# Optimization experiments

Measured on AMD Instinct MI355X. Metric: run time of the kernel, lower is better.

The kernel has to match this reference:

```python
import jax, jax.numpy as jnp
import numpy as np

N = 50000          # nodes
E = 1_000_000      # edges
NODE_DIM = 16
EMB = 64           # embed_dim
OUT = 64           # out_dim per head
EA_DIM = 8         # raw edge_attr_dim
HEADS = 8
SLOPE = 0.01       # leaky_relu default negative slope
LN_EPS = 1e-5


def mlp(x, w, b, g, beta):
    # MLP(in, out): Linear -> LayerNorm -> ReLU (standard block in this repo)
    y = x @ w + b
    mu = jnp.mean(y, axis=-1, keepdims=True)
    var = jnp.var(y, axis=-1, keepdims=True)
    y = (y - mu) / jnp.sqrt(var + LN_EPS) * g + beta
    return jax.nn.relu(y)


def gat_layer(x, ea, src, tgt, W, a):
    """AA_GATlayer forward (dropout = identity at eval).
    x: [N, in], ea: [E, EMB], W: [in, OUT], a: [2*OUT + EMB]."""
    h = x @ W                                  # [N, OUT]
    d = h.shape[1]
    a_src, a_tgt, a_edge = a[:d], a[d:2 * d], a[2 * d:]
    # score = leaky_relu(a @ concat([h_src, h_tgt, ea])) without materializing the concat
    s = jax.nn.leaky_relu(h[src] @ a_src + h[tgt] @ a_tgt + ea @ a_edge, SLOPE)  # [E]
    s = s - jnp.max(s)
    e = jnp.exp(s)
    denom = jax.ops.segment_sum(e, src, num_segments=N)          # [N]
    attn = e / (denom[src] + 1e-16)                              # [E]
    h_prime = jax.ops.segment_sum(h[tgt] * attn[:, None], src, num_segments=N)  # [N, OUT]
    return jax.nn.elu(h_prime)


def setup_inputs() -> dict:
    key = jax.random.key(0)
    ks = jax.random.split(key, 16)
    sc = lambda fan_in: 1.0 / np.sqrt(fan_in)
    inp = {}
    inp["X"] = jax.random.normal(ks[0], (N, NODE_DIM), jnp.float32)
    inp["edge_attr"] = jax.random.normal(ks[1], (E, EA_DIM), jnp.float32)
    inp["edge_index"] = jax.random.randint(ks[2], (2, E), 0, N, jnp.int64)
    inp["matched_car_infra_nodes"] = jax.random.randint(ks[3], (1000,), 0, N, jnp.int64)
    # node_embed MLP params
    inp["w_node"] = jax.random.uniform(ks[4], (NODE_DIM, EMB), jnp.float32, -sc(NODE_DIM), sc(NODE_DIM))
    inp["b_node"] = jnp.zeros((EMB,), jnp.float32)
    inp["g_node"] = jnp.ones((EMB,), jnp.float32)
    inp["beta_node"] = jnp.zeros((EMB,), jnp.float32)
    # edge_attr_embed MLP params
    inp["w_edge"] = jax.random.uniform(ks[5], (EA_DIM, EMB), jnp.float32, -sc(EA_DIM), sc(EA_DIM))
    inp["b_edge"] = jnp.zeros((EMB,), jnp.float32)
    inp["g_edge"] = jnp.ones((EMB,), jnp.float32)
    inp["beta_edge"] = jnp.zeros((EMB,), jnp.float32)
    # 8 GAT heads: W [EMB,OUT], a [2*OUT+EMB]
    inp["gat_W"] = jax.random.uniform(ks[6], (HEADS, EMB, OUT), jnp.float32, -sc(EMB), sc(EMB))
    inp["gat_a"] = jax.random.uniform(ks[7], (HEADS, 2 * OUT + EMB), jnp.float32, -sc(2 * OUT + EMB), sc(2 * OUT + EMB))
    # output GAT layer: W [OUT*HEADS, OUT], a [2*OUT+EMB]
    inp["out_W"] = jax.random.uniform(ks[8], (OUT * HEADS, OUT), jnp.float32, -sc(OUT * HEADS), sc(OUT * HEADS))
    inp["out_a"] = jax.random.uniform(ks[9], (2 * OUT + EMB,), jnp.float32, -sc(2 * OUT + EMB), sc(2 * OUT + EMB))
    return inp


def reference(X, edge_attr, w_node, b_node, g_node, beta_node,
              w_edge, b_edge, g_edge, beta_edge,
              gat_W, gat_a, out_W, out_a,
              edge_index, matched_car_infra_nodes):
    src, tgt = edge_index[0], edge_index[1]
    x = mlp(X, w_node, b_node, g_node, beta_node)                  # [N, EMB]
    ea = mlp(edge_attr, w_edge, b_edge, g_edge, beta_edge)         # [E, EMB]
    heads = [gat_layer(x, ea, src, tgt, gat_W[i], gat_a[i]) for i in range(HEADS)]
    xh = jax.nn.elu(jnp.concatenate(heads, axis=1))                # [N, OUT*HEADS]
    out = gat_layer(xh, ea, src, tgt, out_W, out_a)                # [N, OUT]
    return jax.nn.log_softmax(out, axis=1)
```

## Files before the change

kernel.cpp:

```cpp
#include <hip/hip_runtime.h>
#include <hip/hip_fp16.h>

#define NN 50000
#define EE 1000000
#define HALF 25000
#define EPT 4

typedef _Float16 h8v __attribute__((ext_vector_type(8)));
typedef float    f4a __attribute__((ext_vector_type(4)));
typedef float    f4v __attribute__((ext_vector_type(4)));

__device__ __forceinline__ float wsum(float v){
#pragma unroll
  for(int m=1;m<64;m<<=1) v += __shfl_xor(v,m,64);
  return v;
}
__device__ __forceinline__ unsigned encf(float f){
  unsigned u = __float_as_uint(f);
  return (u & 0x80000000u) ? ~u : (u | 0x80000000u);
}
__device__ __forceinline__ float decf(unsigned u){
  u = (u & 0x80000000u) ? (u & 0x7fffffffu) : ~u;
  return __uint_as_float(u);
}

__global__ __launch_bounds__(256) void zero_k(int* counts, int* cursor, unsigned* mx){
  int i = blockIdx.x*blockDim.x + threadIdx.x;
  if(i < NN){ counts[i] = 0; cursor[i] = 0; }
  if(i < 64) mx[i] = 0u;
}

__global__ __launch_bounds__(64) void cvec_k(const float* __restrict__ gat_W, const float* __restrict__ gat_a,
                                             float* __restrict__ cdir){
  int h = blockIdx.x, k = threadIdx.x;
  const float* W = gat_W + (size_t)h*64*64;
  const float* a = gat_a + (size_t)h*192;
  float cs = 0.f, ct = 0.f;
#pragma unroll
  for(int j=0;j<64;j++){ float wv = W[k*64+j]; cs += wv*a[j]; ct += wv*a[64+j]; }
  cdir[h*64 + k]       = cs;
  cdir[512 + h*64 + k] = ct;
}

__global__ __launch_bounds__(256) void cvtw_k(const float* __restrict__ gat_W, const float* __restrict__ out_W,
                                              __half* __restrict__ WT, __half* __restrict__ OT){
  int h = blockIdx.x; int tid = threadIdx.x;
  for(int idx = tid; idx < 4096; idx += 256){
    int j = idx >> 6, k = idx & 63;
    WT[(size_t)h*4096 + k*64 + j] = __float2half(gat_W[(size_t)h*4096 + j*64 + k]);
    OT[(size_t)h*4096 + k*64 + j] = __float2half(out_W[(size_t)h*4096 + j*64 + k]);
  }
}

__global__ __launch_bounds__(256) void node_mlp(const float* __restrict__ X, const float* __restrict__ w,
                                                const float* __restrict__ b, const float* __restrict__ g,
                                                const float* __restrict__ beta, const float* __restrict__ cdir,
                                                __half* __restrict__ x, float* __restrict__ ps8,
                                                float* __restrict__ pt8){
  int wid  = (blockIdx.x*blockDim.x + threadIdx.x) >> 6;
  int lane = threadIdx.x & 63;
  if(wid >= NN) return;
  float acc = b[lane];
#pragma unroll
  for(int k=0;k<16;k++) acc += X[wid*16+k] * w[k*64+lane];
  float mu  = wsum(acc) * (1.0f/64.0f);
  float d   = acc - mu;
  float var = wsum(d*d) * (1.0f/64.0f);
  float y   = d * rsqrtf(var + 1e-5f) * g[lane] + beta[lane];
  float xv  = fmaxf(y, 0.0f);
  x[(size_t)wid*64 + lane] = __float2half(xv);
#pragma unroll 1
  for(int h=0;h<8;h++){
    float a = wsum(xv * cdir[h*64+lane]);
    float c = wsum(xv * cdir[512 + h*64+lane]);
    if(lane == 0){ ps8[wid*8+h] = a; pt8[wid*8+h] = c; }
  }
}

__global__ __launch_bounds__(256) void hist_k(const int* __restrict__ src, int* __restrict__ counts){
  int e = blockIdx.x*blockDim.x + threadIdx.x;
  if(e < EE){
    int s = src[e];
    if((unsigned)s >= NN) s = 0;
    atomicAdd(&counts[s], 1);
  }
}

__global__ __launch_bounds__(256) void scan1_k(const int* __restrict__ counts, int* __restrict__ bsum){
  int i = blockIdx.x*256 + threadIdx.x;
  int v = (i < NN) ? counts[i] : 0;
  int s = v;
#pragma unroll
  for(int m=1;m<64;m<<=1) s += __shfl_xor(s,m,64);
  __shared__ int sm[4];
  if((threadIdx.x & 63) == 0) sm[threadIdx.x>>6] = s;
  __syncthreads();
  if(threadIdx.x == 0) bsum[blockIdx.x] = sm[0]+sm[1]+sm[2]+sm[3];
}

__global__ __launch_bounds__(256) void scan2_k(const int* __restrict__ bsum, int* __restrict__ bpre,
                                               int* __restrict__ offs){
  const int NB = (NN + 255)/256;
  int t = threadIdx.x;
  __shared__ int sm[256];
  int v = (t < NB) ? bsum[t] : 0;
  sm[t] = v; __syncthreads();
  for(int off=1; off<256; off<<=1){
    int u = (t >= off) ? sm[t-off] : 0;
    __syncthreads();
    sm[t] += u;
    __syncthreads();
  }
  if(t < NB) bpre[t] = sm[t] - v;
  if(t == 0) offs[NN] = EE;
}

__global__ __launch_bounds__(256) void scan3_k(const int* __restrict__ counts, const int* __restrict__ bpre,
                                               int* __restrict__ offs){
  int i = blockIdx.x*256 + threadIdx.x;
  int t = threadIdx.x;
  __shared__ int sm[256];
  int v = (i < NN) ? counts[i] : 0;
  sm[t] = v; __syncthreads();
  for(int off=1; off<256; off<<=1){
    int u = (t >= off) ? sm[t-off] : 0;
    __syncthreads();
    sm[t] += u;
    __syncthreads();
  }
  if(i < NN) offs[i] = bpre[blockIdx.x] + sm[t] - v;
}

__global__ __launch_bounds__(256) void scatter_k(const int* __restrict__ src, const int* __restrict__ tgt,
                                                 const int* __restrict__ offs, int* __restrict__ cursor,
                                                 int* __restrict__ rank, int* __restrict__ tgt_s,
                                                 int* __restrict__ src_s){
  int e = blockIdx.x*blockDim.x + threadIdx.x;
  if(e < EE){
    int s = src[e];
    if((unsigned)s >= NN) s = 0;
    int pos = offs[s] + atomicAdd(&cursor[s], 1);
    rank[e] = pos;
    int t = tgt[e];
    if((unsigned)t >= NN) t = 0;
    tgt_s[pos] = t;
    src_s[pos] = s;
  }
}

__global__ __launch_bounds__(256, 1) void edge_mlp_q(const int* __restrict__ rank, const float* __restrict__ ea,
                                                  const float* __restrict__ w, const float* __restrict__ b,
                                                  const float* __restrict__ g, const float* __restrict__ beta,
                                                  const float* __restrict__ gat_a, const float* __restrict__ out_a,
                                                  __half* __restrict__ q8h, float* __restrict__ q_out,
                                                  unsigned* __restrict__ mx){
  __shared__ float P[64*20];
  __shared__ float smx[4][9];
  int tid = threadIdx.x;
  for(int idx=tid; idx<1280; idx+=256){
    int j = idx/20, c = idx - j*20;
    float v;
    if(c < 8)       v = w[c*64+j];
    else if(c == 8) v = b[j];
    else if(c == 9) v = g[j];
    else if(c ==10) v = beta[j];
    else if(c ==11) v = out_a[128+j];
    else            v = gat_a[(c-12)*192 + 128 + j];
    P[idx] = v;
  }
  __syncthreads();
  int base = blockIdx.x*(256*EPT) + tid;
  float4 ia[EPT], ib[EPT];
  bool  vl[EPT];
#pragma unroll
  for(int k=0;k<EPT;k++){
    int e = base + k*256;
    vl[k] = (e < EE);
    size_t es = vl[k] ? (size_t)e : 0;
    ia[k] = ((const float4*)ea)[es*2];
    ib[k] = ((const float4*)ea)[es*2+1];
  }
  float s1[EPT], s2[EPT];
#pragma unroll
  for(int k=0;k<EPT;k++){ s1[k]=0.f; s2[k]=0.f; }
#pragma unroll 4
  for(int j=0;j<64;j++){
    float4 w0 = *(const float4*)&P[j*20];
    float4 w1 = *(const float4*)&P[j*20+4];
    float4 c4 = *(const float4*)&P[j*20+8];
#pragma unroll
    for(int k=0;k<EPT;k++){
      float acc = c4.x;
      acc = fmaf(ia[k].x,w0.x, fmaf(ia[k].y,w0.y, fmaf(ia[k].z,w0.z, fmaf(ia[k].w,w0.w, acc))));
      acc = fmaf(ib[k].x,w1.x, fmaf(ib[k].y,w1.y, fmaf(ib[k].z,w1.z, fmaf(ib[k].w,w1.w, acc))));
      s1[k] += acc;
      s2[k] = fmaf(acc,acc,s2[k]);
    }
  }
  float mu[EPT], inv[EPT];
#pragma unroll
  for(int k=0;k<EPT;k++){
    mu[k]  = s1[k]*(1.0f/64.0f);
    float var = fmaxf(s2[k]*(1.0f/64.0f) - mu[k]*mu[k], 0.0f);
    inv[k] = rsqrtf(var + 1e-5f);
  }
  float qv[EPT][9];
#pragma unroll
  for(int k=0;k<EPT;k++)
#pragma unroll
    for(int r=0;r<9;r++) qv[k][r]=0.f;
#pragma unroll 4
  for(int j=0;j<64;j++){
    float4 w0 = *(const float4*)&P[j*20];
    float4 w1 = *(const float4*)&P[j*20+4];
    float4 c4 = *(const float4*)&P[j*20+8];
    float4 a0 = *(const float4*)&P[j*20+12];
    float4 a1 = *(const float4*)&P[j*20+16];
#pragma unroll
    for(int k=0;k<EPT;k++){
      float acc = c4.x;
      acc = fmaf(ia[k].x,w0.x, fmaf(ia[k].y,w0.y, fmaf(ia[k].z,w0.z, fmaf(ia[k].w,w0.w, acc))));
      acc = fmaf(ib[k].x,w1.x, fmaf(ib[k].y,w1.y, fmaf(ib[k].z,w1.z, fmaf(ib[k].w,w1.w, acc))));
      float yj = fmaxf(fmaf((acc - mu[k])*inv[k], c4.y, c4.z), 0.0f);
      qv[k][0]=fmaf(yj,a0.x,qv[k][0]); qv[k][1]=fmaf(yj,a0.y,qv[k][1]);
      qv[k][2]=fmaf(yj,a0.z,qv[k][2]); qv[k][3]=fmaf(yj,a0.w,qv[k][3]);
      qv[k][4]=fmaf(yj,a1.x,qv[k][4]); qv[k][5]=fmaf(yj,a1.y,qv[k][5]);
      qv[k][6]=fmaf(yj,a1.z,qv[k][6]); qv[k][7]=fmaf(yj,a1.w,qv[k][7]);
      qv[k][8]=fmaf(yj,c4.w,qv[k][8]);
    }
  }
  float mq[9];
#pragma unroll
  for(int r=0;r<9;r++) mq[r] = -3.0e38f;
#pragma unroll
  for(int k=0;k<EPT;k++){
    if(vl[k]){
      int e = base + k*256;
      int rk = rank[e];
      __half2 p01 = __floats2half2_rn(qv[k][0],qv[k][1]);
      __half2 p23 = __floats2half2_rn(qv[k][2],qv[k][3]);
      __half2 p45 = __floats2half2_rn(qv[k][4],qv[k][5]);
      __half2 p67 = __floats2half2_rn(qv[k][6],qv[k][7]);
      uint4 pk;
      pk.x = *(unsigned*)&p01; pk.y = *(unsigned*)&p23;
      pk.z = *(unsigned*)&p45; pk.w = *(unsigned*)&p67;
      *(uint4*)(q8h + (size_t)rk*8) = pk;
      q_out[rk] = qv[k][8];
#pragma unroll
      for(int r=0;r<9;r++) mq[r] = fmaxf(mq[r], qv[k][r]);
    }
  }
#pragma unroll
  for(int r=0;r<9;r++)
#pragma unroll
    for(int m=1;m<64;m<<=1) mq[r] = fmaxf(mq[r], __shfl_xor(mq[r],m,64));
  int wv = tid>>6, lane = tid&63;
  if(lane == 0){
#pragma unroll
    for(int r=0;r<9;r++) smx[wv][r] = mq[r];
  }
  __syncthreads();
  if(tid < 9){
    float v = fmaxf(fmaxf(smx[0][tid],smx[1][tid]), fmaxf(smx[2][tid],smx[3][tid]));
    atomicMax(&mx[tid], encf(v));
  }
}

__global__ __launch_bounds__(256) void maxp_k(const float* __restrict__ ps8, const float* __restrict__ pt8,
                                              unsigned* __restrict__ mx){
  float m[16];
#pragma unroll
  for(int r=0;r<16;r++) m[r] = -3.0e38f;
  for(int i = blockIdx.x*256 + threadIdx.x; i < NN; i += gridDim.x*256){
    float4 a = ((const float4*)ps8)[(size_t)i*2];
    float4 c = ((const float4*)ps8)[(size_t)i*2+1];
    float4 d = ((const float4*)pt8)[(size_t)i*2];
    float4 e = ((const float4*)pt8)[(size_t)i*2+1];
    m[0]=fmaxf(m[0],a.x); m[1]=fmaxf(m[1],a.y); m[2]=fmaxf(m[2],a.z); m[3]=fmaxf(m[3],a.w);
    m[4]=fmaxf(m[4],c.x); m[5]=fmaxf(m[5],c.y); m[6]=fmaxf(m[6],c.z); m[7]=fmaxf(m[7],c.w);
    m[8]=fmaxf(m[8],d.x); m[9]=fmaxf(m[9],d.y); m[10]=fmaxf(m[10],d.z); m[11]=fmaxf(m[11],d.w);
    m[12]=fmaxf(m[12],e.x); m[13]=fmaxf(m[13],e.y); m[14]=fmaxf(m[14],e.z); m[15]=fmaxf(m[15],e.w);
  }
#pragma unroll
  for(int r=0;r<16;r++)
#pragma unroll
    for(int msk=1;msk<64;msk<<=1) m[r] = fmaxf(m[r], __shfl_xor(m[r],msk,64));
  __shared__ float sm[4][16];
  int wv = threadIdx.x>>6, lane = threadIdx.x&63;
  if(lane == 0){
#pragma unroll
    for(int r=0;r<16;r++) sm[wv][r] = m[r];
  }
  __syncthreads();
  if(threadIdx.x < 16){
    int r = threadIdx.x;
    float v = fmaxf(fmaxf(sm[0][r],sm[1][r]), fmaxf(sm[2][r],sm[3][r]));
    atomicMax(&mx[16+r], encf(v));
  }
}

__global__ __launch_bounds__(256) void maxpo_k(const float* __restrict__ ps_o, const float* __restrict__ pt_o,
                                               unsigned* __restrict__ mx){
  float m0 = -3.0e38f, m1 = -3.0e38f;
  for(int i = blockIdx.x*256 + threadIdx.x; i < NN; i += gridDim.x*256){
    m0 = fmaxf(m0, ps_o[i]); m1 = fmaxf(m1, pt_o[i]);
  }
#pragma unroll
  for(int msk=1;msk<64;msk<<=1){ m0=fmaxf(m0,__shfl_xor(m0,msk,64)); m1=fmaxf(m1,__shfl_xor(m1,msk,64)); }
  __shared__ float sm[4][2];
  int wv = threadIdx.x>>6, lane = threadIdx.x&63;
  if(lane == 0){ sm[wv][0]=m0; sm[wv][1]=m1; }
  __syncthreads();
  if(threadIdx.x < 2){
    int r = threadIdx.x;
    float v = fmaxf(fmaxf(sm[0][r],sm[1][r]), fmaxf(sm[2][r],sm[3][r]));
    atomicMax(&mx[32+r], encf(v));
  }
}

__global__ __launch_bounds__(256) void score_k(const int* __restrict__ src_s, const int* __restrict__ tgt_s,
                                               const float* __restrict__ ps8, const float* __restrict__ pt8,
                                               const unsigned* __restrict__ mx, const __half* __restrict__ q8h,
                                               __half* __restrict__ w8h){
  int i = blockIdx.x*256 + threadIdx.x;
  if(i >= EE) return;
  int s = src_s[i], t = tgt_s[i];
  uint4 rq = *(const uint4*)(q8h + (size_t)i*8);
  float2 q01 = __half22float2(*(const __half2*)&rq.x);
  float2 q23 = __half22float2(*(const __half2*)&rq.y);
  float2 q45 = __half22float2(*(const __half2*)&rq.z);
  float2 q67 = __half22float2(*(const __half2*)&rq.w);
  float4 sa = ((const float4*)ps8)[(size_t)s*2];
  float4 sb = ((const float4*)ps8)[(size_t)s*2+1];
  float4 ta = ((const float4*)pt8)[(size_t)t*2];
  float4 tb = ((const float4*)pt8)[(size_t)t*2+1];
  float sv[8] = {q01.x+sa.x+ta.x, q01.y+sa.y+ta.y, q23.x+sa.z+ta.z, q23.y+sa.w+ta.w,
                 q45.x+sb.x+tb.x, q45.y+sb.y+tb.y, q67.x+sb.z+tb.z, q67.y+sb.w+tb.w};
  float wv[8];
#pragma unroll
  for(int h=0;h<8;h++){
    float B = decf(mx[h]) + decf(mx[16+h]) + decf(mx[24+h]);
    float M = (B > 0.f) ? B : 0.01f*B;
    float x = sv[h];
    x = (x > 0.f) ? x : 0.01f*x;
    wv[h] = __expf(x - M);
  }
  __half2 p01 = __floats2half2_rn(wv[0],wv[1]);
  __half2 p23 = __floats2half2_rn(wv[2],wv[3]);
  __half2 p45 = __floats2half2_rn(wv[4],wv[5]);
  __half2 p67 = __floats2half2_rn(wv[6],wv[7]);
  uint4 pk;
  pk.x = *(unsigned*)&p01; pk.y = *(unsigned*)&p23;
  pk.z = *(unsigned*)&p45; pk.w = *(unsigned*)&p67;
  *(uint4*)(w8h + (size_t)i*8) = pk;
}

__global__ __launch_bounds__(256) void agg_k(const int* __restrict__ offs, const int* __restrict__ tgt_s,
    const __half* __restrict__ w8h, const __half* __restrict__ x, __half* __restrict__ pre, int nbase){
  int wid  = nbase + ((blockIdx.x*blockDim.x + threadIdx.x) >> 6);
  int lane = threadIdx.x & 63;
  int quad = lane >> 4, l16 = lane & 15;
  int b  = offs[wid];
  int e2 = offs[wid+1];
  float  den[8];
  float4 num[8];
#pragma unroll
  for(int h=0;h<8;h++){ den[h] = 0.f; num[h] = make_float4(0.f,0.f,0.f,0.f); }
  for(int i=b+quad; i<e2; i+=4){
    int t = tgt_s[i];
    uint4 rw = *(const uint4*)(w8h + (size_t)i*8);
    float2 w01 = __half22float2(*(const __half2*)&rw.x);
    float2 w23 = __half22float2(*(const __half2*)&rw.y);
    float2 w45 = __half22float2(*(const __half2*)&rw.z);
    float2 w67 = __half22float2(*(const __half2*)&rw.w);
    uint2 raw = *(const uint2*)(x + (size_t)t*64 + l16*4);
    float2 fa = __half22float2(*(const __half2*)&raw.x);
    float2 fb = __half22float2(*(const __half2*)&raw.y);
    float4 xv = make_float4(fa.x, fa.y, fb.x, fb.y);
    float wv[8] = {w01.x,w01.y,w23.x,w23.y, w45.x,w45.y,w67.x,w67.y};
#pragma unroll
    for(int h=0;h<8;h++){
      den[h]   += wv[h];
      num[h].x = fmaf(wv[h],xv.x,num[h].x); num[h].y = fmaf(wv[h],xv.y,num[h].y);
      num[h].z = fmaf(wv[h],xv.z,num[h].z); num[h].w = fmaf(wv[h],xv.w,num[h].w);
    }
  }
#pragma unroll
  for(int h=0;h<8;h++){
    den[h]   += __shfl_xor(den[h],16,64);   den[h]   += __shfl_xor(den[h],32,64);
    num[h].x += __shfl_xor(num[h].x,16,64); num[h].x += __shfl_xor(num[h].x,32,64);
    num[h].y += __shfl_xor(num[h].y,16,64); num[h].y += __shfl_xor(num[h].y,32,64);
    num[h].z += __shfl_xor(num[h].z,16,64); num[h].z += __shfl_xor(num[h].z,32,64);
    num[h].w += __shfl_xor(num[h].w,16,64); num[h].w += __shfl_xor(num[h].w,32,64);
  }
  __half* dst = pre + (size_t)(wid - nbase)*512;
#pragma unroll
  for(int k=0;k<2;k++){
    int h = 2*quad + k;
    float invd = (den[h] > 0.f) ? 1.0f/den[h] : 0.f;
    __half2 h0 = __floats2half2_rn(num[h].x*invd, num[h].y*invd);
    __half2 h1 = __floats2half2_rn(num[h].z*invd, num[h].w*invd);
    uint2 pk; pk.x = *(unsigned*)&h0; pk.y = *(unsigned*)&h1;
    *(uint2*)(dst + h*64 + l16*4) = pk;
  }
}

__global__ __launch_bounds__(256) void transform_mfma(const __half* __restrict__ pre,
                                                      const __half* __restrict__ WT,
                                                      const __half* __restrict__ OT,
                                                      float* __restrict__ h2p,
                                                      int nbase, int cn){
  __shared__ __half zl[4*16*64];
  int tid = threadIdx.x;
  int w  = tid >> 6, l = tid & 63;
  int lr = l & 15, lg = l >> 4;
  int n0 = blockIdx.x * 64;
  int g  = blockIdx.y;
  h2p += (size_t)g * NN * 64;
  int gn  = n0 + w*16 + lr;
  int gnr = (gn < cn) ? gn : 0;
  __half* zw = zl + w*1024;
  f4a out[4];
#pragma unroll
  for(int i=0;i<4;i++){ out[i][0]=0.f; out[i][1]=0.f; out[i][2]=0.f; out[i][3]=0.f; }
#pragma unroll 1
  for(int hh=0; hh<4; hh++){
    int h = g*4 + hh;
    h8v a1_0 = *(const h8v*)(pre + (size_t)gnr*512 + h*64 + 0*32 + lg*8);
    h8v a1_1 = *(const h8v*)(pre + (size_t)gnr*512 + h*64 + 1*32 + lg*8);
    f4a zacc[4];
#pragma unroll
    for(int nt=0; nt<4; nt++){ zacc[nt][0]=0.f; zacc[nt][1]=0.f; zacc[nt][2]=0.f; zacc[nt][3]=0.f; }
    const __half* WTh = WT + (size_t)h*4096;
#pragma unroll
    for(int nt=0; nt<4; nt++){
      h8v b0 = *(const h8v*)(WTh + (nt*16 + lr)*64 + 0*32 + lg*8);
      h8v b1 = *(const h8v*)(WTh + (nt*16 + lr)*64 + 1*32 + lg*8);
      zacc[nt] = __builtin_amdgcn_mfma_f32_16x16x32_f16(a1_0, b0, zacc[nt], 0, 0, 0);
      zacc[nt] = __builtin_amdgcn_mfma_f32_16x16x32_f16(a1_1, b1, zacc[nt], 0, 0, 0);
    }
#pragma unroll
    for(int nt=0; nt<4; nt++){
#pragma unroll
      for(int r=0; r<4; r++){
        float v = zacc[nt][r];
        float z = (v > 0.f) ? v : expm1f(v);
        z = (z > 0.f) ? z : expm1f(z);
        int rho = lg*4 + r;
        int c   = nt*16 + lr;
        int pc  = (((c>>3) ^ (rho&7))<<3) | (c&7);
        zw[rho*64 + pc] = __float2half(z);
      }
    }
    const __half* OTh = OT + (size_t)h*4096;
#pragma unroll
    for(int ks=0; ks<2; ks++){
      int Gp = (lg + 4*ks) ^ (lr & 7);
      h8v a2 = *(const h8v*)(zw + lr*64 + Gp*8);
#pragma unroll
      for(int nt=0; nt<4; nt++){
        h8v b2 = *(const h8v*)(OTh + (nt*16 + lr)*64 + ks*32 + lg*8);
        out[nt] = __builtin_amdgcn_mfma_f32_16x16x32_f16(a2, b2, out[nt], 0, 0, 0);
      }
    }
  }
#pragma unroll
  for(int nt=0; nt<4; nt++){
#pragma unroll
    for(int r=0; r<4; r++){
      int grow = n0 + w*16 + lg*4 + r;
      if(grow < cn) h2p[(size_t)(nbase + grow)*64 + nt*16 + lr] = out[nt][r];
    }
  }
}

__global__ __launch_bounds__(256) void finalize_po(const float* __restrict__ p0, const float* __restrict__ p1,
                                                   const float* __restrict__ out_a, __half* __restrict__ h2f,
                                                   float* __restrict__ ps_o, float* __restrict__ pt_o){
  int wid  = (blockIdx.x*blockDim.x + threadIdx.x) >> 6;
  int lane = threadIdx.x & 63;
  if(wid >= NN) return;
  float v = p0[(size_t)wid*64 + lane] + p1[(size_t)wid*64 + lane];
  float ps = wsum(v * out_a[lane]);
  float pt = wsum(v * out_a[64+lane]);
  if(lane == 0){ ps_o[wid] = ps; pt_o[wid] = pt; }
  h2f[(size_t)wid*64 + lane] = __float2half(v);
}

__global__ __launch_bounds__(256) void agg_out(const int* __restrict__ offs, const int* __restrict__ tgt_s,
                                               const float* __restrict__ q_out, const float* __restrict__ ps_o,
                                               const float* __restrict__ pt_o, const unsigned* __restrict__ mx,
                                               const __half* __restrict__ h2f, float* __restrict__ dout){
  int wid  = (blockIdx.x*blockDim.x + threadIdx.x) >> 6;
  int lane = threadIdx.x & 63;
  if(wid >= NN) return;
  int quad = lane >> 4, l16 = lane & 15;
  int b  = offs[wid];
  int e2 = offs[wid+1];
  float B = decf(mx[8]) + decf(mx[32]) + decf(mx[33]);
  float M = (B > 0.f) ? B : 0.01f*B;
  float pso = ps_o[wid];
  float4 num = make_float4(0.f,0.f,0.f,0.f);
  float den = 0.f;
  for(int i=b+quad; i<e2; i+=4){
    int t = tgt_s[i];
    float sv = q_out[i] + pso + pt_o[t];
    sv = (sv > 0.f) ? sv : 0.01f*sv;
    float w = __expf(sv - M);
    uint2 raw = *(const uint2*)(h2f + (size_t)t*64 + l16*4);
    float2 fa = __half22float2(*(const __half2*)&raw.x);
    float2 fb = __half22float2(*(const __half2*)&raw.y);
    den += w;
    num.x = fmaf(w,fa.x,num.x); num.y = fmaf(w,fa.y,num.y);
    num.z = fmaf(w,fb.x,num.z); num.w = fmaf(w,fb.y,num.w);
  }
  den   += __shfl_xor(den,16,64);   den   += __shfl_xor(den,32,64);
  num.x += __shfl_xor(num.x,16,64); num.x += __shfl_xor(num.x,32,64);
  num.y += __shfl_xor(num.y,16,64); num.y += __shfl_xor(num.y,32,64);
  num.z += __shfl_xor(num.z,16,64); num.z += __shfl_xor(num.z,32,64);
  num.w += __shfl_xor(num.w,16,64); num.w += __shfl_xor(num.w,32,64);
  float inv = (den > 0.f) ? 1.0f/den : 0.f;
  float z[4];
  float mloc = -3.0e38f;
#pragma unroll
  for(int k=0;k<4;k++){
    float hp = ((&num.x)[k]) * inv;
    z[k] = (hp > 0.f) ? hp : expm1f(hp);
    mloc = fmaxf(mloc, z[k]);
  }
#pragma unroll
  for(int msk=1; msk<16; msk<<=1) mloc = fmaxf(mloc, __shfl_xor(mloc,msk,64));
  float ssum = 0.f;
#pragma unroll
  for(int k=0;k<4;k++) ssum += __expf(z[k] - mloc);
#pragma unroll
  for(int msk=1; msk<16; msk<<=1) ssum += __shfl_xor(ssum,msk,64);
  float lse = mloc + logf(ssum);
  if(quad == 0){
    f4v o; o.x = z[0]-lse; o.y = z[1]-lse; o.z = z[2]-lse; o.w = z[3]-lse;
    __builtin_nontemporal_store(o, (f4v*)(dout + (size_t)wid*64 + l16*4));
  }
}

extern "C" void kernel_launch(void* const* d_in, const int* in_sizes, int n_in,
                              void* d_out, int out_size, void* d_ws, size_t ws_size,
                              hipStream_t stream) {
  const float* X         = (const float*)d_in[0];
  const float* edge_attr = (const float*)d_in[1];
  const int*   edge_index= (const int*)d_in[2];
  const float* w_node    = (const float*)d_in[4];
  const float* b_node    = (const float*)d_in[5];
  const float* g_node    = (const float*)d_in[6];
  const float* beta_node = (const float*)d_in[7];
  const float* w_edge    = (const float*)d_in[8];
  const float* b_edge    = (const float*)d_in[9];
  const float* g_edge    = (const float*)d_in[10];
  const float* beta_edge = (const float*)d_in[11];
  const float* gat_W     = (const float*)d_in[12];
  const float* gat_a     = (const float*)d_in[13];
  const float* out_W     = (const float*)d_in[14];
  const float* out_a     = (const float*)d_in[15];
  float* dout = (float*)d_out;

  const int* src = edge_index;
  const int* tgt = edge_index + EE;

  char* base = (char*)d_ws;
  size_t off = 0;
  auto take = [&](size_t bytes)->char*{ char* p = base + off; off += (bytes + 31) & ~(size_t)31; return p; };
  int*      counts = (int*)     take((size_t)NN*4);
  int*      cursor = (int*)     take((size_t)NN*4);
  int*      offs   = (int*)     take((size_t)(NN+1)*4);
  int*      bsum   = (int*)     take(256*4);
  int*      bpre   = (int*)     take(256*4);
  unsigned* mx     = (unsigned*)take(64*4);
  float*    ps_o   = (float*)   take((size_t)NN*4);
  float*    pt_o   = (float*)   take((size_t)NN*4);
  float*    cdir   = (float*)   take(1024*4);
  int*      rank   = (int*)     take((size_t)EE*4);
  int*      tgt_s  = (int*)     take((size_t)EE*4);
  int*      src_s  = (int*)     take((size_t)EE*4);
  float*    ps8    = (float*)   take((size_t)NN*8*4);
  float*    pt8    = (float*)   take((size_t)NN*8*4);
  __half*   xh     = (__half*)  take((size_t)NN*64*2);
  __half*   h2fh   = (__half*)  take((size_t)NN*64*2);
  __half*   WT16   = (__half*)  take((size_t)8*4096*2);
  __half*   OT16   = (__half*)  take((size_t)8*4096*2);
  float*    h2p    = (float*)   take((size_t)2*NN*64*4);
  __half*   q8h    = (__half*)  take((size_t)EE*8*2);
  __half*   w8h    = (__half*)  take((size_t)EE*8*2);
  float*    q_out  = (float*)   take((size_t)EE*4);
  __half*   pre    = (__half*)  take((size_t)HALF*512*2);

  const int NBLK_N  = (NN*64 + 255)/256;
  const int NBLK_E  = (EE + 255)/256;
  const int NBLK_EM = (EE + 256*EPT - 1)/(256*EPT);
  const int NBLK_S  = (NN + 255)/256;
  const int NBLK_A  = HALF/4;
  const int NBLK_T  = (HALF + 63)/64;

  zero_k   <<<NBLK_S, 256, 0, stream>>>(counts, cursor, mx);
  cvec_k   <<<8,       64, 0, stream>>>(gat_W, gat_a, cdir);
  cvtw_k   <<<8,      256, 0, stream>>>(gat_W, out_W, WT16, OT16);
  node_mlp <<<NBLK_N, 256, 0, stream>>>(X, w_node, b_node, g_node, beta_node, cdir, xh, ps8, pt8);
  hist_k   <<<NBLK_E, 256, 0, stream>>>(src, counts);
  scan1_k  <<<NBLK_S, 256, 0, stream>>>(counts, bsum);
  scan2_k  <<<1,      256, 0, stream>>>(bsum, bpre, offs);
  scan3_k  <<<NBLK_S, 256, 0, stream>>>(counts, bpre, offs);
  scatter_k<<<NBLK_E, 256, 0, stream>>>(src, tgt, offs, cursor, rank, tgt_s, src_s);
  edge_mlp_q<<<NBLK_EM,256, 0, stream>>>(rank, edge_attr, w_edge, b_edge, g_edge, beta_edge,
                                        gat_a, out_a, q8h, q_out, mx);
  maxp_k   <<<128,    256, 0, stream>>>(ps8, pt8, mx);
  score_k  <<<NBLK_E, 256, 0, stream>>>(src_s, tgt_s, ps8, pt8, mx, q8h, w8h);

  for(int half=0; half<2; half++){
    int nbase = half*HALF;
    agg_k<<<NBLK_A, 256, 0, stream>>>(offs, tgt_s, w8h, xh, pre, nbase);
    dim3 tg((unsigned)NBLK_T, 2);
    transform_mfma<<<tg, 256, 0, stream>>>(pre, WT16, OT16, h2p, nbase, HALF);
  }

  finalize_po<<<NBLK_N, 256, 0, stream>>>(h2p, h2p + (size_t)NN*64, out_a, h2fh, ps_o, pt_o);
  maxpo_k    <<<128,  256, 0, stream>>>(ps_o, pt_o, mx);
  agg_out    <<<NBLK_N,256, 0, stream>>>(offs, tgt_s, q_out, ps_o, pt_o, mx, h2fh, dout);
}
```

Before: 686.8 us.

## Merge prep kernels, fuse node MLP with histogram, single-block scan, unsplit aggregation

Folds the zero, cvec and weight-transpose kernels into one prep kernel. It also fuses node_mlp with the edge histogram in a single launch and replaces the three-pass scan with one 1024-thread block scan. The two-half agg/transform loop becomes one pass over all nodes, using a full-size pre buffer, and edge_mlp_q launch bounds are relaxed to allow two blocks per CU. Together these cut launch count and serial gaps, at the cost of a larger workspace (about 51MB for pre) and a scan that runs on a single block.

```diff
diff --git a/kernel.cpp b/kernel.cpp
--- a/kernel.cpp
+++ b/kernel.cpp
@@ -3,7 +3,6 @@
 
 #define NN 50000
 #define EE 1000000
-#define HALF 25000
 #define EPT 4
 
 typedef _Float16 h8v __attribute__((ext_vector_type(8)));
@@ -24,40 +23,50 @@
   return __uint_as_float(u);
 }
 
-__global__ __launch_bounds__(256) void zero_k(int* counts, int* cursor, unsigned* mx){
-  int i = blockIdx.x*blockDim.x + threadIdx.x;
+__global__ __launch_bounds__(256) void prep_k(int* counts, int* cursor, unsigned* mx,
+                                              const float* __restrict__ gat_W, const float* __restrict__ gat_a,
+                                              const float* __restrict__ out_W, const float* __restrict__ out_a,
+                                              float* __restrict__ cdir, __half* __restrict__ WT,
+                                              __half* __restrict__ OT){
+  int i = blockIdx.x*256 + threadIdx.x;
   if(i < NN){ counts[i] = 0; cursor[i] = 0; }
   if(i < 64) mx[i] = 0u;
-}
-
-__global__ __launch_bounds__(64) void cvec_k(const float* __restrict__ gat_W, const float* __restrict__ gat_a,
-                                             float* __restrict__ cdir){
-  int h = blockIdx.x, k = threadIdx.x;
-  const float* W = gat_W + (size_t)h*64*64;
-  const float* a = gat_a + (size_t)h*192;
-  float cs = 0.f, ct = 0.f;
-#pragma unroll
-  for(int j=0;j<64;j++){ float wv = W[k*64+j]; cs += wv*a[j]; ct += wv*a[64+j]; }
-  cdir[h*64 + k]       = cs;
-  cdir[512 + h*64 + k] = ct;
-}
-
-__global__ __launch_bounds__(256) void cvtw_k(const float* __restrict__ gat_W, const float* __restrict__ out_W,
-                                              __half* __restrict__ WT, __half* __restrict__ OT){
-  int h = blockIdx.x; int tid = threadIdx.x;
-  for(int idx = tid; idx < 4096; idx += 256){
-    int j = idx >> 6, k = idx & 63;
-    WT[(size_t)h*4096 + k*64 + j] = __float2half(gat_W[(size_t)h*4096 + j*64 + k]);
-    OT[(size_t)h*4096 + k*64 + j] = __float2half(out_W[(size_t)h*4096 + j*64 + k]);
-  }
-}
-
-__global__ __launch_bounds__(256) void node_mlp(const float* __restrict__ X, const float* __restrict__ w,
-                                                const float* __restrict__ b, const float* __restrict__ g,
-                                                const float* __restrict__ beta, const float* __restrict__ cdir,
-                                                __half* __restrict__ x, float* __restrict__ ps8,
-                                                float* __restrict__ pt8){
-  int wid  = (blockIdx.x*blockDim.x + threadIdx.x) >> 6;
+  if(blockIdx.x < 8){
+    int h = blockIdx.x, tid = threadIdx.x;
+    if(tid < 64){
+      const float* W = gat_W + (size_t)h*4096;
+      const float* a = gat_a + (size_t)h*192;
+      float cs = 0.f, ct = 0.f;
+#pragma unroll
+      for(int j=0;j<64;j++){ float wv = W[tid*64+j]; cs += wv*a[j]; ct += wv*a[64+j]; }
+      cdir[h*64 + tid]       = cs;
+      cdir[512 + h*64 + tid] = ct;
+    }
+    for(int idx = tid; idx < 4096; idx += 256){
+      int j = idx >> 6, k = idx & 63;
+      WT[(size_t)h*4096 + k*64 + j] = __float2half(gat_W[(size_t)h*4096 + j*64 + k]);
+      OT[(size_t)h*4096 + k*64 + j] = __float2half(out_W[(size_t)h*4096 + j*64 + k]);
+    }
+  }
+}
+
+__global__ __launch_bounds__(256) void node_hist_k(const float* __restrict__ X, const float* __restrict__ w,
+                                                   const float* __restrict__ b, const float* __restrict__ g,
+                                                   const float* __restrict__ beta, const float* __restrict__ cdir,
+                                                   __half* __restrict__ x, float* __restrict__ ps8,
+                                                   float* __restrict__ pt8,
+                                                   const int* __restrict__ src, int* __restrict__ counts){
+  const int NB_N = (NN*64 + 255)/256;
+  if(blockIdx.x >= NB_N){
+    int e = (blockIdx.x - NB_N)*256 + threadIdx.x;
+    if(e < EE){
+      int s = src[e];
+      if((unsigned)s >= NN) s = 0;
+      atomicAdd(&counts[s], 1);
+    }
+    return;
+  }
+  int wid  = (blockIdx.x*256 + threadIdx.x) >> 6;
   int lane = threadIdx.x & 63;
   if(wid >= NN) return;
   float acc = b[lane];
@@ -77,58 +86,33 @@
   }
 }
 
-__global__ __launch_bounds__(256) void hist_k(const int* __restrict__ src, int* __restrict__ counts){
-  int e = blockIdx.x*blockDim.x + threadIdx.x;
-  if(e < EE){
-    int s = src[e];
-    if((unsigned)s >= NN) s = 0;
-    atomicAdd(&counts[s], 1);
-  }
-}
-
-__global__ __launch_bounds__(256) void scan1_k(const int* __restrict__ counts, int* __restrict__ bsum){
-  int i = blockIdx.x*256 + threadIdx.x;
-  int v = (i < NN) ? counts[i] : 0;
-  int s = v;
-#pragma unroll
-  for(int m=1;m<64;m<<=1) s += __shfl_xor(s,m,64);
-  __shared__ int sm[4];
-  if((threadIdx.x & 63) == 0) sm[threadIdx.x>>6] = s;
-  __syncthreads();
-  if(threadIdx.x == 0) bsum[blockIdx.x] = sm[0]+sm[1]+sm[2]+sm[3];
-}
-
-__global__ __launch_bounds__(256) void scan2_k(const int* __restrict__ bsum, int* __restrict__ bpre,
-                                               int* __restrict__ offs){
-  const int NB = (NN + 255)/256;
+#define SCH 49
+__global__ __launch_bounds__(1024) void scan_k(const int* __restrict__ counts, int* __restrict__ offs){
+  __shared__ int sm[1024];
   int t = threadIdx.x;
-  __shared__ int sm[256];
-  int v = (t < NB) ? bsum[t] : 0;
-  sm[t] = v; __syncthreads();
-  for(int off=1; off<256; off<<=1){
+  int base = t*SCH;
+  int loc[SCH];
+  int sum = 0;
+#pragma unroll
+  for(int i=0;i<SCH;i++){
+    int idx = base+i;
+    int v = (idx < NN) ? counts[idx] : 0;
+    loc[i] = sum; sum += v;
+  }
+  sm[t] = sum; __syncthreads();
+  for(int off=1; off<1024; off<<=1){
     int u = (t >= off) ? sm[t-off] : 0;
     __syncthreads();
     sm[t] += u;
     __syncthreads();
   }
-  if(t < NB) bpre[t] = sm[t] - v;
+  int ex = (t == 0) ? 0 : sm[t-1];
+#pragma unroll
+  for(int i=0;i<SCH;i++){
+    int idx = base+i;
+    if(idx < NN) offs[idx] = ex + loc[i];
+  }
   if(t == 0) offs[NN] = EE;
-}
-
-__global__ __launch_bounds__(256) void scan3_k(const int* __restrict__ counts, const int* __restrict__ bpre,
-                                               int* __restrict__ offs){
-  int i = blockIdx.x*256 + threadIdx.x;
-  int t = threadIdx.x;
-  __shared__ int sm[256];
-  int v = (i < NN) ? counts[i] : 0;
-  sm[t] = v; __syncthreads();
-  for(int off=1; off<256; off<<=1){
-    int u = (t >= off) ? sm[t-off] : 0;
-    __syncthreads();
-    sm[t] += u;
-    __syncthreads();
-  }
-  if(i < NN) offs[i] = bpre[blockIdx.x] + sm[t] - v;
 }
 
 __global__ __launch_bounds__(256) void scatter_k(const int* __restrict__ src, const int* __restrict__ tgt,
@@ -148,7 +132,7 @@
   }
 }
 
-__global__ __launch_bounds__(256, 1) void edge_mlp_q(const int* __restrict__ rank, const float* __restrict__ ea,
+__global__ __launch_bounds__(256, 2) void edge_mlp_q(const int* __restrict__ rank, const float* __restrict__ ea,
                                                   const float* __restrict__ w, const float* __restrict__ b,
                                                   const float* __restrict__ g, const float* __restrict__ beta,
                                                   const float* __restrict__ gat_a, const float* __restrict__ out_a,
@@ -356,8 +340,8 @@
 }
 
 __global__ __launch_bounds__(256) void agg_k(const int* __restrict__ offs, const int* __restrict__ tgt_s,
-    const __half* __restrict__ w8h, const __half* __restrict__ x, __half* __restrict__ pre, int nbase){
-  int wid  = nbase + ((blockIdx.x*blockDim.x + threadIdx.x) >> 6);
+    const __half* __restrict__ w8h, const __half* __restrict__ x, __half* __restrict__ pre){
+  int wid  = (blockIdx.x*blockDim.x + threadIdx.x) >> 6;
   int lane = threadIdx.x & 63;
   int quad = lane >> 4, l16 = lane & 15;
   int b  = offs[wid];
@@ -393,7 +377,7 @@
     num[h].z += __shfl_xor(num[h].z,16,64); num[h].z += __shfl_xor(num[h].z,32,64);
     num[h].w += __shfl_xor(num[h].w,16,64); num[h].w += __shfl_xor(num[h].w,32,64);
   }
-  __half* dst = pre + (size_t)(wid - nbase)*512;
+  __half* dst = pre + (size_t)wid*512;
 #pragma unroll
   for(int k=0;k<2;k++){
     int h = 2*quad + k;
@@ -408,8 +392,7 @@
 __global__ __launch_bounds__(256) void transform_mfma(const __half* __restrict__ pre,
                                                       const __half* __restrict__ WT,
                                                       const __half* __restrict__ OT,
-                                                      float* __restrict__ h2p,
-                                                      int nbase, int cn){
+                                                      float* __restrict__ h2p){
   __shared__ __half zl[4*16*64];
   int tid = threadIdx.x;
   int w  = tid >> 6, l = tid & 63;
@@ -418,7 +401,7 @@
   int g  = blockIdx.y;
   h2p += (size_t)g * NN * 64;
   int gn  = n0 + w*16 + lr;
-  int gnr = (gn < cn) ? gn : 0;
+  int gnr = (gn < NN) ? gn : 0;
   __half* zw = zl + w*1024;
   f4a out[4];
 #pragma unroll
@@ -469,7 +452,7 @@
 #pragma unroll
     for(int r=0; r<4; r++){
       int grow = n0 + w*16 + lg*4 + r;
-      if(grow < cn) h2p[(size_t)(nbase + grow)*64 + nt*16 + lr] = out[nt][r];
+      if(grow < NN) h2p[(size_t)grow*64 + nt*16 + lr] = out[nt][r];
     }
   }
 }
@@ -571,8 +554,6 @@
   int*      counts = (int*)     take((size_t)NN*4);
   int*      cursor = (int*)     take((size_t)NN*4);
   int*      offs   = (int*)     take((size_t)(NN+1)*4);
-  int*      bsum   = (int*)     take(256*4);
-  int*      bpre   = (int*)     take(256*4);
   unsigned* mx     = (unsigned*)take(64*4);
   float*    ps_o   = (float*)   take((size_t)NN*4);
   float*    pt_o   = (float*)   take((size_t)NN*4);
@@ -590,36 +571,30 @@
   __half*   q8h    = (__half*)  take((size_t)EE*8*2);
   __half*   w8h    = (__half*)  take((size_t)EE*8*2);
   float*    q_out  = (float*)   take((size_t)EE*4);
-  __half*   pre    = (__half*)  take((size_t)HALF*512*2);
+  __half*   pre    = (__half*)  take((size_t)NN*512*2);
 
   const int NBLK_N  = (NN*64 + 255)/256;
   const int NBLK_E  = (EE + 255)/256;
   const int NBLK_EM = (EE + 256*EPT - 1)/(256*EPT);
   const int NBLK_S  = (NN + 255)/256;
-  const int NBLK_A  = HALF/4;
-  const int NBLK_T  = (HALF + 63)/64;
-
-  zero_k   <<<NBLK_S, 256, 0, stream>>>(counts, cursor, mx);
-  cvec_k   <<<8,       64, 0, stream>>>(gat_W, gat_a, cdir);
-  cvtw_k   <<<8,      256, 0, stream>>>(gat_W, out_W, WT16, OT16);
-  node_mlp <<<NBLK_N, 256, 0, stream>>>(X, w_node, b_node, g_node, beta_node, cdir, xh, ps8, pt8);
-  hist_k   <<<NBLK_E, 256, 0, stream>>>(src, counts);
-  scan1_k  <<<NBLK_S, 256, 0, stream>>>(counts, bsum);
-  scan2_k  <<<1,      256, 0, stream>>>(bsum, bpre, offs);
-  scan3_k  <<<NBLK_S, 256, 0, stream>>>(counts, bpre, offs);
-  scatter_k<<<NBLK_E, 256, 0, stream>>>(src, tgt, offs, cursor, rank, tgt_s, src_s);
-  edge_mlp_q<<<NBLK_EM,256, 0, stream>>>(rank, edge_attr, w_edge, b_edge, g_edge, beta_edge,
-                                        gat_a, out_a, q8h, q_out, mx);
-  maxp_k   <<<128,    256, 0, stream>>>(ps8, pt8, mx);
-  score_k  <<<NBLK_E, 256, 0, stream>>>(src_s, tgt_s, ps8, pt8, mx, q8h, w8h);
-
-  for(int half=0; half<2; half++){
-    int nbase = half*HALF;
-    agg_k<<<NBLK_A, 256, 0, stream>>>(offs, tgt_s, w8h, xh, pre, nbase);
+  const int NBLK_A  = (NN + 3)/4;
+  const int NBLK_T  = (NN + 63)/64;
+
+  prep_k     <<<NBLK_S, 256, 0, stream>>>(counts, cursor, mx, gat_W, gat_a, out_W, out_a,
+                                          cdir, WT16, OT16);
+  node_hist_k<<<NBLK_N + NBLK_E, 256, 0, stream>>>(X, w_node, b_node, g_node, beta_node, cdir,
+                                                   xh, ps8, pt8, src, counts);
+  scan_k     <<<1,     1024, 0, stream>>>(counts, offs);
+  scatter_k  <<<NBLK_E, 256, 0, stream>>>(src, tgt, offs, cursor, rank, tgt_s, src_s);
+  edge_mlp_q <<<NBLK_EM,256, 0, stream>>>(rank, edge_attr, w_edge, b_edge, g_edge, beta_edge,
+                                          gat_a, out_a, q8h, q_out, mx);
+  maxp_k     <<<128,    256, 0, stream>>>(ps8, pt8, mx);
+  score_k    <<<NBLK_E, 256, 0, stream>>>(src_s, tgt_s, ps8, pt8, mx, q8h, w8h);
+  agg_k      <<<NBLK_A, 256, 0, stream>>>(offs, tgt_s, w8h, xh, pre);
+  {
     dim3 tg((unsigned)NBLK_T, 2);
-    transform_mfma<<<tg, 256, 0, stream>>>(pre, WT16, OT16, h2p, nbase, HALF);
-  }
-
+    transform_mfma<<<tg, 256, 0, stream>>>(pre, WT16, OT16, h2p);
+  }
   finalize_po<<<NBLK_N, 256, 0, stream>>>(h2p, h2p + (size_t)NN*64, out_a, h2fh, ps_o, pt_o);
   maxpo_k    <<<128,  256, 0, stream>>>(ps_o, pt_o, mx);
   agg_out    <<<NBLK_N,256, 0, stream>>>(offs, tgt_s, q_out, ps_o, pt_o, mx, h2fh, dout);
```

Result: no change. 680.9 us (-0.9%).
